# Kernel tuning notes

Measured on AMD Instinct MI355X. Metric: run time of the kernel, lower is better.

The kernel has to match this reference:

```python
import jax, jax.numpy as jnp
import numpy as np

SIZE = 128
RATIO = 0.5

def setup_inputs() -> dict:
    key = jax.random.key(0)
    k1, k2, k3 = jax.random.split(key, 3)
    B, D, K = 16, 256, 18
    assp_features = jax.random.normal(k1, (B, D, SIZE, SIZE), dtype=jnp.float32)
    prototypes = jax.random.normal(k2, (B, K, D), dtype=jnp.float32)
    n_samp = int(SIZE * SIZE * RATIO)
    # sample without replacement, matching np.random.choice(replace=False)
    random_indices = jax.random.permutation(k3, SIZE * SIZE)[:n_samp].astype(jnp.int64)
    return {"assp_features": assp_features, "prototypes": prototypes,
            "random_indices": random_indices}

def reference(assp_features, prototypes, random_indices):
    # assp_features: [B, D, H, W], prototypes: [B, K, D], random_indices: [N]
    size = assp_features.shape[-1]
    x = random_indices // size  # [N]
    y = random_indices % size   # [N]
    f = assp_features[:, :, x, y]            # [B, D, N] gathered pixel features
    # squared L2 distances [B, N, K]; argmin of ||p-f||_2 == argmin of squared dist
    p2 = jnp.sum(prototypes * prototypes, axis=-1)       # [B, K]
    f2 = jnp.sum(f * f, axis=1)                          # [B, N]
    cross = jnp.einsum('bdn,bkd->bnk', f, prototypes)    # [B, N, K]
    d2 = p2[:, None, :] - 2.0 * cross + f2[:, :, None]
    idx = jnp.argmin(d2, axis=-1)                        # [B, N]
    nearest = jnp.take_along_axis(prototypes, idx[..., None], axis=1)  # [B, N, D]
    out = assp_features.at[:, :, x, y].set(jnp.swapaxes(nearest, 1, 2))
    return out
```

## Files before the change

### kernel.cpp

```cpp
#include <hip/hip_runtime.h>

constexpr int B = 16;
constexpr int D = 256;
constexpr int K = 18;
constexpr int SZ = 128;
constexpr int S = SZ * SZ;
constexpr int N = S / 2;

__global__ __launch_bounds__(256) void prep2_kernel(
    const float* __restrict__ proto,
    const int* __restrict__ idx,
    unsigned char* __restrict__ mask,
    double* __restrict__ p2) {
  const int blk = blockIdx.x;
  if (blk < 32) {
    mask[idx[blk * 256 + threadIdx.x]] = 1;
  } else {
    const int row  = (blk - 32) * 4 + (threadIdx.x >> 6);
    const int lane = threadIdx.x & 63;
    const float4 v = *(const float4*)(proto + (size_t)row * D + lane * 4);
    double s = (double)v.x * (double)v.x + (double)v.y * (double)v.y
             + (double)v.z * (double)v.z + (double)v.w * (double)v.w;
#pragma unroll
    for (int off = 1; off < 64; off <<= 1)
      s += __shfl_xor(s, off, 64);
    if (lane == 0) p2[row] = s;
  }
}

__global__ __launch_bounds__(256) void argmin_kernel(
    const float* __restrict__ assp,
    const float* __restrict__ proto,
    const double* __restrict__ p2,
    signed char* __restrict__ table) {
  __shared__ double spd[D][K];

  const int b     = blockIdx.x & 15;
  const int chunk = blockIdx.x >> 4;

  const float* pb = proto + (size_t)b * K * D;
  for (int i = threadIdx.x; i < K * D; i += 256)
    spd[i & 255][i >> 8] = (double)pb[i];
  __syncthreads();

  const int sA = chunk * 512 + threadIdx.x;
  const float* fA = assp + (size_t)b * D * S + sA;

  double accA[K], accB[K];
#pragma unroll
  for (int k = 0; k < K; ++k) { accA[k] = 0.0; accB[k] = 0.0; }

  for (int d = 0; d < D; d += 8) {
    float va[8], vb[8];
#pragma unroll
    for (int j = 0; j < 8; ++j) {
      va[j] = fA[(size_t)(d + j) * S];
      vb[j] = fA[(size_t)(d + j) * S + 256];
    }
#pragma unroll
    for (int j = 0; j < 8; ++j) {
      const double a  = (double)va[j];
      const double bb = (double)vb[j];
      const double* pr = spd[d + j];
#pragma unroll
      for (int k = 0; k < K; ++k) {
        const double pk = pr[k];
        accA[k] += a * pk;
        accB[k] += bb * pk;
      }
    }
  }

  const double* p2b = p2 + (size_t)b * K;
  double bestA = 1e300, bestB = 1e300;
  int kA = 0, kB = 0;
#pragma unroll
  for (int k = 0; k < K; ++k) {
    const double dA = p2b[k] - 2.0 * accA[k];
    const double dB = p2b[k] - 2.0 * accB[k];
    if (dA < bestA) { bestA = dA; kA = k; }
    if (dB < bestB) { bestB = dB; kB = k; }
  }
  table[(size_t)b * S + sA]       = (signed char)kA;
  table[(size_t)b * S + sA + 256] = (signed char)kB;
}

__global__ __launch_bounds__(256) void scatter_kernel(
    const float* __restrict__ assp,
    const float* __restrict__ proto,
    const signed char* __restrict__ table,
    const unsigned char* __restrict__ mask,
    float* __restrict__ out) {
  const int d  = 255 - (blockIdx.x >> 4);
  const int b  = blockIdx.x & 15;
  const int bd = b * D + d;

  __shared__ float sp[K];
  if (threadIdx.x < K)
    sp[threadIdx.x] = proto[((size_t)b * K + threadIdx.x) * D + d];
  __syncthreads();

  const signed char* tb = table + (size_t)b * S;
  const float4* in4 = (const float4*)(assp + (size_t)bd * S);
  float4* out4 = (float4*)(out + (size_t)bd * S);

#pragma unroll
  for (int it = 0; it < S / 4 / 256; ++it) {
    const int i = it * 256 + threadIdx.x;
    char4 t, m;
    *(int*)&t = ((const int*)tb)[i];
    *(int*)&m = ((const int*)mask)[i];
    float4 v = in4[i];
    if (m.x) v.x = sp[(int)t.x];
    if (m.y) v.y = sp[(int)t.y];
    if (m.z) v.z = sp[(int)t.z];
    if (m.w) v.w = sp[(int)t.w];
    out4[i] = v;
  }
}

extern "C" void kernel_launch(void* const* d_in, const int* in_sizes, int n_in,
                              void* d_out, int out_size, void* d_ws, size_t ws_size,
                              hipStream_t stream) {
  const float* assp  = (const float*)d_in[0];
  const float* proto = (const float*)d_in[1];
  const int*   idx   = (const int*)d_in[2];
  float* out = (float*)d_out;

  signed char*   table = (signed char*)d_ws;
  unsigned char* mask  = (unsigned char*)d_ws + (size_t)B * S;
  double*        p2    = (double*)((char*)d_ws + (size_t)B * S + S);

  hipMemsetAsync(mask, 0, S, stream);
  prep2_kernel<<<104, 256, 0, stream>>>(proto, idx, mask, p2);
  argmin_kernel<<<B * (S / 512), 256, 0, stream>>>(assp, proto, p2, table);
  scatter_kernel<<<B * D, 256, 0, stream>>>(assp, proto, table, mask, out);
}
```

Before: 187.9 us.

## Fuse argmin and scatter into one kernel staging features in shared memory

```diff
diff --git a/kernel.cpp b/kernel.cpp
--- a/kernel.cpp
+++ b/kernel.cpp
@@ -6,16 +6,18 @@
 constexpr int SZ = 128;
 constexpr int S = SZ * SZ;
 constexpr int N = S / 2;
+constexpr int PB = 64;
 
-__global__ __launch_bounds__(256) void prep2_kernel(
+__global__ __launch_bounds__(256) void prep_kernel(
     const float* __restrict__ proto,
     const int* __restrict__ idx,
     unsigned char* __restrict__ mask,
-    double* __restrict__ p2) {
+    double* __restrict__ p2,
+    double* __restrict__ p64) {
   const int blk = blockIdx.x;
   if (blk < 32) {
     mask[idx[blk * 256 + threadIdx.x]] = 1;
-  } else {
+  } else if (blk < 104) {
     const int row  = (blk - 32) * 4 + (threadIdx.x >> 6);
     const int lane = threadIdx.x & 63;
     const float4 v = *(const float4*)(proto + (size_t)row * D + lane * 4);
@@ -25,97 +27,89 @@
     for (int off = 1; off < 64; off <<= 1)
       s += __shfl_xor(s, off, 64);
     if (lane == 0) p2[row] = s;
+  } else {
+    const int e = (blk - 104) * 256 + threadIdx.x;
+    const int b = e / (D * K);
+    const int r = e - b * (D * K);
+    const int d = r / K;
+    const int k = r - d * K;
+    p64[e] = (double)proto[((size_t)b * K + k) * D + d];
   }
 }
 
-__global__ __launch_bounds__(256) void argmin_kernel(
+__global__ __launch_bounds__(256) void fused_kernel(
     const float* __restrict__ assp,
     const float* __restrict__ proto,
+    const double* __restrict__ p64,
     const double* __restrict__ p2,
-    signed char* __restrict__ table) {
-  __shared__ double spd[D][K];
+    const unsigned char* __restrict__ mask,
+    float* __restrict__ out) {
+  __shared__ float  fs[D][PB];
+  __shared__ double red[4][6][PB];
 
   const int b     = blockIdx.x & 15;
   const int chunk = blockIdx.x >> 4;
+  const int pos0  = chunk * PB;
+  const int w     = __builtin_amdgcn_readfirstlane(threadIdx.x >> 6);
+  const int lane  = threadIdx.x & 63;
 
-  const float* pb = proto + (size_t)b * K * D;
-  for (int i = threadIdx.x; i < K * D; i += 256)
-    spd[i & 255][i >> 8] = (double)pb[i];
+  const float* fin = assp + (size_t)(b * D) * S + pos0;
+  {
+    const int dr = threadIdx.x >> 4;
+    const int p4 = threadIdx.x & 15;
+    for (int i = 0; i < 16; i += 4) {
+      float4 v[4];
+#pragma unroll
+      for (int j = 0; j < 4; ++j)
+        v[j] = *(const float4*)(fin + (size_t)((i + j) * 16 + dr) * S + p4 * 4);
+#pragma unroll
+      for (int j = 0; j < 4; ++j)
+        *(float4*)&fs[(i + j) * 16 + dr][p4 * 4] = v[j];
+    }
+  }
   __syncthreads();
 
-  const int sA = chunk * 512 + threadIdx.x;
-  const float* fA = assp + (size_t)b * D * S + sA;
+  double acc[K];
+#pragma unroll
+  for (int k = 0; k < K; ++k) acc[k] = 0.0;
+  const double* pw = p64 + ((size_t)b * D + w * 64) * K;
+  for (int i = 0; i < 64; ++i) {
+    const double f = (double)fs[w * 64 + i][lane];
+    const double* pr = pw + i * K;
+#pragma unroll
+    for (int k = 0; k < K; ++k) acc[k] += f * pr[k];
+  }
 
-  double accA[K], accB[K];
+  const double* p2b = p2 + b * K;
+  double best = 1e300;
+  int kstar = 0;
+  for (int c = 0; c < 3; ++c) {
+    __syncthreads();
 #pragma unroll
-  for (int k = 0; k < K; ++k) { accA[k] = 0.0; accB[k] = 0.0; }
-
-  for (int d = 0; d < D; d += 8) {
-    float va[8], vb[8];
+    for (int j = 0; j < 6; ++j) red[w][j][lane] = acc[c * 6 + j];
+    __syncthreads();
 #pragma unroll
-    for (int j = 0; j < 8; ++j) {
-      va[j] = fA[(size_t)(d + j) * S];
-      vb[j] = fA[(size_t)(d + j) * S + 256];
-    }
-#pragma unroll
-    for (int j = 0; j < 8; ++j) {
-      const double a  = (double)va[j];
-      const double bb = (double)vb[j];
-      const double* pr = spd[d + j];
-#pragma unroll
-      for (int k = 0; k < K; ++k) {
-        const double pk = pr[k];
-        accA[k] += a * pk;
-        accB[k] += bb * pk;
-      }
+    for (int j = 0; j < 6; ++j) {
+      const double s = ((red[0][j][lane] + red[1][j][lane]) + red[2][j][lane])
+                     + red[3][j][lane];
+      const double d2 = p2b[c * 6 + j] - 2.0 * s;
+      if (d2 < best) { best = d2; kstar = c * 6 + j; }
     }
   }
 
-  const double* p2b = p2 + (size_t)b * K;
-  double bestA = 1e300, bestB = 1e300;
-  int kA = 0, kB = 0;
-#pragma unroll
-  for (int k = 0; k < K; ++k) {
-    const double dA = p2b[k] - 2.0 * accA[k];
-    const double dB = p2b[k] - 2.0 * accB[k];
-    if (dA < bestA) { bestA = dA; kA = k; }
-    if (dB < bestB) { bestB = dB; kB = k; }
-  }
-  table[(size_t)b * S + sA]       = (signed char)kA;
-  table[(size_t)b * S + sA + 256] = (signed char)kB;
-}
-
-__global__ __launch_bounds__(256) void scatter_kernel(
-    const float* __restrict__ assp,
-    const float* __restrict__ proto,
-    const signed char* __restrict__ table,
-    const unsigned char* __restrict__ mask,
-    float* __restrict__ out) {
-  const int d  = 255 - (blockIdx.x >> 4);
-  const int b  = blockIdx.x & 15;
-  const int bd = b * D + d;
-
-  __shared__ float sp[K];
-  if (threadIdx.x < K)
-    sp[threadIdx.x] = proto[((size_t)b * K + threadIdx.x) * D + d];
-  __syncthreads();
-
-  const signed char* tb = table + (size_t)b * S;
-  const float4* in4 = (const float4*)(assp + (size_t)bd * S);
-  float4* out4 = (float4*)(out + (size_t)bd * S);
-
-#pragma unroll
-  for (int it = 0; it < S / 4 / 256; ++it) {
-    const int i = it * 256 + threadIdx.x;
-    char4 t, m;
-    *(int*)&t = ((const int*)tb)[i];
-    *(int*)&m = ((const int*)mask)[i];
-    float4 v = in4[i];
-    if (m.x) v.x = sp[(int)t.x];
-    if (m.y) v.y = sp[(int)t.y];
-    if (m.z) v.z = sp[(int)t.z];
-    if (m.w) v.w = sp[(int)t.w];
-    out4[i] = v;
+  const int m = mask[pos0 + lane];
+  float* op = out + ((size_t)(b * D + w * 64)) * S + pos0;
+  const float* pkf = proto + ((size_t)(b * K + kstar)) * D + w * 64;
+  for (int i = 0; i < 64; i += 4) {
+    const float4 pv = *(const float4*)(pkf + i);
+    const float f0 = fs[w * 64 + i + 0][lane];
+    const float f1 = fs[w * 64 + i + 1][lane];
+    const float f2 = fs[w * 64 + i + 2][lane];
+    const float f3 = fs[w * 64 + i + 3][lane];
+    op[(size_t)(i + 0) * S + lane] = m ? pv.x : f0;
+    op[(size_t)(i + 1) * S + lane] = m ? pv.y : f1;
+    op[(size_t)(i + 2) * S + lane] = m ? pv.z : f2;
+    op[(size_t)(i + 3) * S + lane] = m ? pv.w : f3;
   }
 }
 
@@ -127,12 +121,11 @@
   const int*   idx   = (const int*)d_in[2];
   float* out = (float*)d_out;
 
-  signed char*   table = (signed char*)d_ws;
-  unsigned char* mask  = (unsigned char*)d_ws + (size_t)B * S;
-  double*        p2    = (double*)((char*)d_ws + (size_t)B * S + S);
+  unsigned char* mask = (unsigned char*)d_ws;
+  double*        p2   = (double*)((char*)d_ws + S);
+  double*        p64  = (double*)((char*)d_ws + S + (size_t)B * K * 8);
 
   hipMemsetAsync(mask, 0, S, stream);
-  prep2_kernel<<<104, 256, 0, stream>>>(proto, idx, mask, p2);
-  argmin_kernel<<<B * (S / 512), 256, 0, stream>>>(assp, proto, p2, table);
-  scatter_kernel<<<B * D, 256, 0, stream>>>(assp, proto, table, mask, out);
+  prep_kernel<<<392, 256, 0, stream>>>(proto, idx, mask, p2, p64);
+  fused_kernel<<<B * (S / PB), 256, 0, stream>>>(assp, proto, p64, p2, mask, out);
 }
```

Result: slower. 212.5 us (+13.1%).

## Double-buffer features into LDS via async global_load_lds and split K across lane pairs

Applied to the files above, without the earlier changes.

```diff
diff --git a/kernel.cpp b/kernel.cpp
--- a/kernel.cpp
+++ b/kernel.cpp
@@ -3,9 +3,19 @@
 constexpr int B = 16;
 constexpr int D = 256;
 constexpr int K = 18;
+constexpr int KH = 9;
 constexpr int SZ = 128;
 constexpr int S = SZ * SZ;
 constexpr int N = S / 2;
+constexpr int PB = 512;
+constexpr int TP = 4;
+constexpr int NT = D / TP;
+
+__device__ __forceinline__ void load_lds16(const float* g, float* l) {
+  __builtin_amdgcn_global_load_lds(
+      (const __attribute__((address_space(1))) void*)g,
+      (__attribute__((address_space(3))) void*)l, 16, 0, 0);
+}
 
 __global__ __launch_bounds__(256) void prep2_kernel(
     const float* __restrict__ proto,
@@ -28,61 +38,99 @@
   }
 }
 
-__global__ __launch_bounds__(256) void argmin_kernel(
+__global__ __launch_bounds__(256, 2) void argmin_kernel(
     const float* __restrict__ assp,
     const float* __restrict__ proto,
     const double* __restrict__ p2,
     signed char* __restrict__ table) {
   __shared__ double spd[D][K];
+  __shared__ float  fs[2][TP][PB];
 
   const int b     = blockIdx.x & 15;
   const int chunk = blockIdx.x >> 4;
+  const int bpos0 = chunk * PB;
+  const int tid   = threadIdx.x;
+  const int lane  = tid & 63;
+  const int wv    = tid >> 6;
+  const int kh    = lane & 1;
+  const int pair  = lane >> 1;
+  const int lpos  = wv * 128 + pair * 4;
 
-  const float* pb = proto + (size_t)b * K * D;
-  for (int i = threadIdx.x; i < K * D; i += 256)
-    spd[i & 255][i >> 8] = (double)pb[i];
+  const float* pbr = proto + (size_t)b * K * D;
+  for (int i = tid; i < K * D; i += 256)
+    spd[i & 255][i >> 8] = (double)pbr[i];
+
+  const float* gbase = assp + (size_t)b * D * S + bpos0;
+
+  {
+    const float* src = gbase + (size_t)wv * S + lane * 4;
+    load_lds16(src,       &fs[0][wv][0]);
+    load_lds16(src + 256, &fs[0][wv][256]);
+  }
   __syncthreads();
 
-  const int sA = chunk * 512 + threadIdx.x;
-  const float* fA = assp + (size_t)b * D * S + sA;
+  double acc[4][KH];
+#pragma unroll
+  for (int jp = 0; jp < 4; ++jp)
+#pragma unroll
+    for (int j = 0; j < KH; ++j) acc[jp][j] = 0.0;
 
-  double accA[K], accB[K];
-#pragma unroll
-  for (int k = 0; k < K; ++k) { accA[k] = 0.0; accB[k] = 0.0; }
-
-  for (int d = 0; d < D; d += 8) {
-    float va[8], vb[8];
-#pragma unroll
-    for (int j = 0; j < 8; ++j) {
-      va[j] = fA[(size_t)(d + j) * S];
-      vb[j] = fA[(size_t)(d + j) * S + 256];
+  int buf = 0;
+  for (int t = 0; t < NT; ++t) {
+    if (t + 1 < NT) {
+      const float* src = gbase + (size_t)((t + 1) * TP + wv) * S + lane * 4;
+      load_lds16(src,       &fs[buf ^ 1][wv][0]);
+      load_lds16(src + 256, &fs[buf ^ 1][wv][256]);
     }
 #pragma unroll
-    for (int j = 0; j < 8; ++j) {
-      const double a  = (double)va[j];
-      const double bb = (double)vb[j];
-      const double* pr = spd[d + j];
+    for (int dj = 0; dj < TP; ++dj) {
+      const int d = t * TP + dj;
+      const float4 f4 = *(const float4*)&fs[buf][dj][lpos];
+      const double f0 = (double)f4.x, f1 = (double)f4.y;
+      const double f2 = (double)f4.z, f3 = (double)f4.w;
+      const double* pr = &spd[d][kh * KH];
 #pragma unroll
-      for (int k = 0; k < K; ++k) {
-        const double pk = pr[k];
-        accA[k] += a * pk;
-        accB[k] += bb * pk;
+      for (int j = 0; j < KH; ++j) {
+        const double pk = pr[j];
+        acc[0][j] += f0 * pk;
+        acc[1][j] += f1 * pk;
+        acc[2][j] += f2 * pk;
+        acc[3][j] += f3 * pk;
       }
     }
+    __syncthreads();
+    buf ^= 1;
   }
 
-  const double* p2b = p2 + (size_t)b * K;
-  double bestA = 1e300, bestB = 1e300;
-  int kA = 0, kB = 0;
+  const double* p2h = p2 + (size_t)b * K + kh * KH;
+  int kst[4];
 #pragma unroll
-  for (int k = 0; k < K; ++k) {
-    const double dA = p2b[k] - 2.0 * accA[k];
-    const double dB = p2b[k] - 2.0 * accB[k];
-    if (dA < bestA) { bestA = dA; kA = k; }
-    if (dB < bestB) { bestB = dB; kB = k; }
+  for (int jp = 0; jp < 4; ++jp) {
+    double bb = 1e300;
+    int bj = 0;
+#pragma unroll
+    for (int j = 0; j < KH; ++j) {
+      const double d2 = p2h[j] - 2.0 * acc[jp][j];
+      if (d2 < bb) { bb = d2; bj = j; }
+    }
+    const int myk = kh * KH + bj;
+    const double ob = __shfl_xor(bb, 1, 64);
+    const int    ok = __shfl_xor(myk, 1, 64);
+    const double bLow  = kh ? ob  : bb;
+    const int    kLow  = kh ? ok  : myk;
+    const double bHigh = kh ? bb  : ob;
+    const int    kHigh = kh ? myk : ok;
+    kst[jp] = (bLow <= bHigh) ? kLow : kHigh;
   }
-  table[(size_t)b * S + sA]       = (signed char)kA;
-  table[(size_t)b * S + sA + 256] = (signed char)kB;
+
+  if (kh == 0) {
+    uchar4 kk;
+    kk.x = (unsigned char)kst[0];
+    kk.y = (unsigned char)kst[1];
+    kk.z = (unsigned char)kst[2];
+    kk.w = (unsigned char)kst[3];
+    *(uchar4*)&table[(size_t)b * S + bpos0 + lpos] = kk;
+  }
 }
 
 __global__ __launch_bounds__(256) void scatter_kernel(
@@ -133,6 +181,6 @@
 
   hipMemsetAsync(mask, 0, S, stream);
   prep2_kernel<<<104, 256, 0, stream>>>(proto, idx, mask, p2);
-  argmin_kernel<<<B * (S / 512), 256, 0, stream>>>(assp, proto, p2, table);
+  argmin_kernel<<<B * (S / PB), 256, 0, stream>>>(assp, proto, p2, table);
   scatter_kernel<<<B * D, 256, 0, stream>>>(assp, proto, table, mask, out);
 }
```

New measurement: 207.2 us. 10.3% more time.
